# Optimization experiments

Measured on AMD Instinct MI355X. Metric: run time of the kernel, lower is better.

Reference implementation:

```python
import jax, jax.numpy as jnp
import numpy as np

B, L = 1024, 256
D = 64        # neighbor_interaction_feat_dim
TD = 100      # time_encoder.dim
NUM_NODES = 20000


def setup_inputs() -> dict:
    key = jax.random.key(0)
    ks = jax.random.split(key, 12)
    return {
        "src_ids": jax.random.randint(ks[0], (B, L), 0, NUM_NODES),
        "dst_ids": jax.random.randint(ks[1], (B, L), 0, NUM_NODES),
        "src_times": jax.random.uniform(ks[2], (B, L), jnp.float32),
        "dst_times": jax.random.uniform(ks[3], (B, L), jnp.float32),
        "node_times": jax.random.uniform(ks[4], (B,), jnp.float32) + 1.0,
        "num_nodes": NUM_NODES,
        # LTF time encoder: cos(t * w + b)
        "w_time": jax.random.normal(ks[5], (TD,), jnp.float32),
        "b_time": jax.random.normal(ks[6], (TD,), jnp.float32) * 0.1,
        # time_to_scalar: Linear(TD, 1)
        "w_ts": jax.random.normal(ks[7], (TD,), jnp.float32) / np.sqrt(TD),
        "b_ts": jnp.zeros((), jnp.float32),
        # MLP: Linear(1, D) -> ReLU -> Linear(D, D)
        "w1": jax.random.normal(ks[8], (D,), jnp.float32),
        "b1": jax.random.normal(ks[9], (D,), jnp.float32) * 0.1,
        "w2": jax.random.normal(ks[10], (D, D), jnp.float32) / np.sqrt(D),
        "b2": jax.random.normal(ks[11], (D,), jnp.float32) * 0.1,
    }


def _histogram(ids, num_nodes):
    # per-row count of each node id, with id==0 treated as padding (count 0)
    b = ids.shape[0]
    mask = (ids != 0).astype(jnp.float32)
    hist = jnp.zeros((b, num_nodes), jnp.float32)
    return hist.at[jnp.arange(b)[:, None], ids].add(mask)


def _time_weight(time_diff, w_time, b_time, w_ts, b_ts):
    # LTF: cos(t*w + b) -> Linear(TD,1) -> sigmoid, all fused elementwise+dot
    feat = jnp.cos(time_diff[..., None] * w_time + b_time)  # (B,L,TD)
    return jax.nn.sigmoid(feat @ w_ts + b_ts)               # (B,L)


def _mlp_sum(weighted_counts, w1, b1, w2, b2):
    # weighted_counts: (B,L,2) scalar counts -> Linear(1,D) -> ReLU -> Linear(D,D), sum over axis 2
    h = jax.nn.relu(weighted_counts[..., None] * w1 + b1)   # (B,L,2,D)
    return (h @ w2 + b2).sum(axis=2)                        # (B,L,D)


def reference(src_ids, dst_ids, src_times, dst_times, node_times, num_nodes,
              w_time, b_time, w_ts, b_ts, w1, b1, w2, b2):
    hist_src = _histogram(src_ids, num_nodes)  # (B,N)
    hist_dst = _histogram(dst_ids, num_nodes)

    c_ss = jnp.take_along_axis(hist_src, src_ids, axis=1)
    c_sd = jnp.take_along_axis(hist_dst, src_ids, axis=1)
    c_ds = jnp.take_along_axis(hist_src, dst_ids, axis=1)
    c_dd = jnp.take_along_axis(hist_dst, dst_ids, axis=1)

    src_counts = jnp.stack([c_ss, c_sd], axis=2)  # (B,L,2)
    dst_counts = jnp.stack([c_ds, c_dd], axis=2)

    src_w = _time_weight(node_times[:, None] - src_times, w_time, b_time, w_ts, b_ts)
    dst_w = _time_weight(node_times[:, None] - dst_times, w_time, b_time, w_ts, b_ts)

    src_features = _mlp_sum(src_counts * src_w[..., None], w1, b1, w2, b2)
    dst_features = _mlp_sum(dst_counts * dst_w[..., None], w1, b1, w2, b2)
    return src_features, dst_features
```

## Files before the change

kernel.cpp:

```cpp
#include <hip/hip_runtime.h>

#define BB 1024
#define LL 256
#define DD 64
#define TDIM 100

typedef _Float16 half8_t __attribute__((ext_vector_type(8)));
typedef float f32x4 __attribute__((ext_vector_type(4)));

__global__ __launch_bounds__(256, 3) void tni_kernel(
    const int* __restrict__ src_ids, const int* __restrict__ dst_ids,
    const float* __restrict__ src_tm, const float* __restrict__ dst_tm,
    const float* __restrict__ node_tm,
    const float* __restrict__ w_time, const float* __restrict__ b_time,
    const float* __restrict__ w_ts, const float* __restrict__ b_ts,
    const float* __restrict__ w1, const float* __restrict__ b1,
    const float* __restrict__ w2, const float* __restrict__ b2,
    float* __restrict__ out)
{
    __shared__ half8_t W2v[DD*8];
    __shared__ half8_t Gv[LL*8];

    const int t    = threadIdx.x;
    const int b    = blockIdx.x >> 1;
    const int side = blockIdx.x & 1;

    {
        _Float16* w2s = (_Float16*)W2v;
        #pragma unroll
        for (int i = 0; i < 16; ++i) {
            int idx = t + 256*i;
            int e = idx >> 6, d = idx & 63;
            int chunk = (e >> 3) ^ (d & 7);
            w2s[d*64 + (chunk << 3) + (e & 7)] = (_Float16)w2[idx];
        }
    }

    const int*   my_ids = side ? dst_ids : src_ids;
    const float* my_tms = side ? dst_tm  : src_tm;
    const int   my_id = my_ids[b*LL + t];
    const float my_tm = my_tms[b*LL + t];

    const int4* sr4 = (const int4*)(src_ids + b*LL);
    const int4* dr4 = (const int4*)(dst_ids + b*LL);
    int c1 = 0, c2 = 0;
    #pragma unroll 8
    for (int j = 0; j < LL/4; ++j) {
        int4 a  = sr4[j];
        int4 dd = dr4[j];
        c1 += (a.x==my_id) + (a.y==my_id) + (a.z==my_id) + (a.w==my_id);
        c2 += (dd.x==my_id) + (dd.y==my_id) + (dd.z==my_id) + (dd.w==my_id);
    }
    if (my_id == 0) { c1 = 0; c2 = 0; }

    const float inv2pi = 0.15915494309189535f;
    float td = node_tm[b] - my_tm;
    float z  = b_ts[0];
    #pragma unroll 4
    for (int k = 0; k < TDIM; ++k) {
        float u = fmaf(td, w_time[k], b_time[k]);
        float r = __builtin_amdgcn_fractf(u * inv2pi);
        z = fmaf(__builtin_amdgcn_cosf(r), w_ts[k], z);
    }
    float ee  = __builtin_amdgcn_exp2f(-1.44269504f * z);
    float wgt = __builtin_amdgcn_rcpf(1.0f + ee);
    float c1w = (float)c1 * wgt;
    float c2w = (float)c2 * wgt;

    #pragma unroll
    for (int c = 0; c < 8; ++c) {
        half8_t h;
        #pragma unroll
        for (int j = 0; j < 8; ++j) {
            float w1e = w1[c*8 + j], b1e = b1[c*8 + j];
            float g = fmaxf(fmaf(c1w, w1e, b1e), 0.f)
                    + fmaxf(fmaf(c2w, w1e, b1e), 0.f);
            h[j] = (_Float16)g;
        }
        Gv[t*8 + (c ^ (t & 7))] = h;
    }
    __syncthreads();

    const int w    = t >> 6;
    const int l    = t & 63;
    const int quad = l >> 4;
    const int lr   = l & 15;

    f32x4 acc[4][4];
    #pragma unroll
    for (int mt = 0; mt < 4; ++mt)
        #pragma unroll
        for (int nt = 0; nt < 4; ++nt) {
            f32x4 zz = {0.f, 0.f, 0.f, 0.f};
            acc[mt][nt] = zz;
        }

    #pragma unroll
    for (int s = 0; s < 2; ++s) {
        const int c = s*4 + quad;
        half8_t bfr[4], afr[4];
        #pragma unroll
        for (int nt = 0; nt < 4; ++nt) {
            int n = nt*16 + lr;
            bfr[nt] = W2v[n*8 + (c ^ (n & 7))];
        }
        #pragma unroll
        for (int mt = 0; mt < 4; ++mt) {
            int row = w*64 + mt*16 + lr;
            afr[mt] = Gv[row*8 + (c ^ (row & 7))];
        }
        #pragma unroll
        for (int mt = 0; mt < 4; ++mt)
            #pragma unroll
            for (int nt = 0; nt < 4; ++nt)
                acc[mt][nt] = __builtin_amdgcn_mfma_f32_16x16x32_f16(
                    afr[mt], bfr[nt], acc[mt][nt], 0, 0, 0);
    }

    float b2v[4];
    #pragma unroll
    for (int nt = 0; nt < 4; ++nt)
        b2v[nt] = 2.f * b2[nt*16 + lr];

    const int obase = side * (BB*LL*DD) + b * (LL*DD);
    #pragma unroll
    for (int mt = 0; mt < 4; ++mt) {
        #pragma unroll
        for (int r = 0; r < 4; ++r) {
            int pos = w*64 + mt*16 + quad*4 + r;
            #pragma unroll
            for (int nt = 0; nt < 4; ++nt) {
                out[obase + pos*DD + nt*16 + lr] = acc[mt][nt][r] + b2v[nt];
            }
        }
    }
}

extern "C" void kernel_launch(void* const* d_in, const int* in_sizes, int n_in,
                              void* d_out, int out_size, void* d_ws, size_t ws_size,
                              hipStream_t stream) {
    const int* src_ids = (const int*)d_in[0];
    const int* dst_ids = (const int*)d_in[1];
    const float* src_tm  = (const float*)d_in[2];
    const float* dst_tm  = (const float*)d_in[3];
    const float* node_tm = (const float*)d_in[4];
    const float* w_time = (const float*)d_in[6];
    const float* b_time = (const float*)d_in[7];
    const float* w_ts   = (const float*)d_in[8];
    const float* b_ts   = (const float*)d_in[9];
    const float* w1     = (const float*)d_in[10];
    const float* b1     = (const float*)d_in[11];
    const float* w2     = (const float*)d_in[12];
    const float* b2     = (const float*)d_in[13];
    float* out = (float*)d_out;

    tni_kernel<<<dim3(BB*2), dim3(256), 0, stream>>>(
        src_ids, dst_ids, src_tm, dst_tm, node_tm,
        w_time, b_time, w_ts, b_ts, w1, b1, w2, b2, out);
}
```

Measured before the change: 187.4 us.

## Replace MLP matmul with precomputed piecewise-linear breakpoint table lookup

```diff
diff --git a/kernel.cpp b/kernel.cpp
--- a/kernel.cpp
+++ b/kernel.cpp
@@ -5,36 +5,79 @@
 #define DD 64
 #define TDIM 100
 
-typedef _Float16 half8_t __attribute__((ext_vector_type(8)));
-typedef float f32x4 __attribute__((ext_vector_type(4)));
+#define BIG 3.0e38f
+#define TBL_OFF 256
 
-__global__ __launch_bounds__(256, 3) void tni_kernel(
+__global__ void tni_prep(const float* __restrict__ w1, const float* __restrict__ b1,
+                         const float* __restrict__ w2, const float* __restrict__ b2,
+                         float* __restrict__ ws)
+{
+    __shared__ float tauS[DD];
+    __shared__ int   vS[DD];
+    __shared__ float bpS[DD];
+    __shared__ int   beS[DD];
+
+    const int t = threadIdx.x;
+    float we = w1[t], be = b1[t];
+    float tau = -be / we;
+    int valid = (we != 0.0f) && (tau > 0.0f) && (tau < 1.0e3f);
+    tauS[t] = tau; vS[t] = valid;
+    bpS[t] = BIG;  beS[t] = 0;
+    __syncthreads();
+
+    int rank = 0;
+    for (int j = 0; j < DD; ++j) {
+        if (vS[j] && (tauS[j] < tau || (tauS[j] == tau && j < t))) rank++;
+    }
+    __syncthreads();
+    if (valid) { bpS[rank] = tau; beS[rank] = t; }
+    __syncthreads();
+
+    ws[t] = bpS[t];
+
+    float c0 = fminf(bpS[0] * 0.5f, 1.0f);
+    float A  = 0.0f;
+    float Bv = b2[t];
+    for (int e = 0; e < DD; ++e) {
+        float w1e = w1[e], b1e = b1[e];
+        float w2r = w2[e*DD + t];
+        if (fmaf(c0, w1e, b1e) > 0.0f) {
+            A  = fmaf(w1e, w2r, A);
+            Bv = fmaf(b1e, w2r, Bv);
+        }
+    }
+    float* tbl = ws + TBL_OFF;
+    tbl[(t>>2)*8     + (t&3)] = A;
+    tbl[(t>>2)*8 + 4 + (t&3)] = Bv;
+    for (int i = 0; i < DD; ++i) {
+        if (bpS[i] > 1.0e38f) break;
+        int   e   = beS[i];
+        float w1e = w1[e], b1e = b1[e];
+        float w2r = w2[e*DD + t];
+        float s   = (w1e > 0.0f) ? 1.0f : -1.0f;
+        A  = fmaf(s*w1e, w2r, A);
+        Bv = fmaf(s*b1e, w2r, Bv);
+        tbl[(i+1)*128 + (t>>2)*8     + (t&3)] = A;
+        tbl[(i+1)*128 + (t>>2)*8 + 4 + (t&3)] = Bv;
+    }
+}
+
+__global__ __launch_bounds__(256, 6) void tni_main(
     const int* __restrict__ src_ids, const int* __restrict__ dst_ids,
     const float* __restrict__ src_tm, const float* __restrict__ dst_tm,
     const float* __restrict__ node_tm,
     const float* __restrict__ w_time, const float* __restrict__ b_time,
     const float* __restrict__ w_ts, const float* __restrict__ b_ts,
-    const float* __restrict__ w1, const float* __restrict__ b1,
-    const float* __restrict__ w2, const float* __restrict__ b2,
-    float* __restrict__ out)
+    const float* __restrict__ ws, float* __restrict__ out)
 {
-    __shared__ half8_t W2v[DD*8];
-    __shared__ half8_t Gv[LL*8];
+    __shared__ float  bpS[DD];
+    __shared__ float4 cv[LL];
 
     const int t    = threadIdx.x;
     const int b    = blockIdx.x >> 1;
     const int side = blockIdx.x & 1;
 
-    {
-        _Float16* w2s = (_Float16*)W2v;
-        #pragma unroll
-        for (int i = 0; i < 16; ++i) {
-            int idx = t + 256*i;
-            int e = idx >> 6, d = idx & 63;
-            int chunk = (e >> 3) ^ (d & 7);
-            w2s[d*64 + (chunk << 3) + (e & 7)] = (_Float16)w2[idx];
-        }
-    }
+    if (t < DD) bpS[t] = ws[t];
 
     const int*   my_ids = side ? dst_ids : src_ids;
     const float* my_tms = side ? dst_tm  : src_tm;
@@ -44,7 +87,7 @@
     const int4* sr4 = (const int4*)(src_ids + b*LL);
     const int4* dr4 = (const int4*)(dst_ids + b*LL);
     int c1 = 0, c2 = 0;
-    #pragma unroll 8
+    #pragma unroll 2
     for (int j = 0; j < LL/4; ++j) {
         int4 a  = sr4[j];
         int4 dd = dr4[j];
@@ -67,72 +110,42 @@
     float c1w = (float)c1 * wgt;
     float c2w = (float)c2 * wgt;
 
-    #pragma unroll
-    for (int c = 0; c < 8; ++c) {
-        half8_t h;
-        #pragma unroll
-        for (int j = 0; j < 8; ++j) {
-            float w1e = w1[c*8 + j], b1e = b1[c*8 + j];
-            float g = fmaxf(fmaf(c1w, w1e, b1e), 0.f)
-                    + fmaxf(fmaf(c2w, w1e, b1e), 0.f);
-            h[j] = (_Float16)g;
-        }
-        Gv[t*8 + (c ^ (t & 7))] = h;
-    }
     __syncthreads();
 
-    const int w    = t >> 6;
-    const int l    = t & 63;
-    const int quad = l >> 4;
-    const int lr   = l & 15;
+    int k1 = 0, k2 = 0;
+    #pragma unroll
+    for (int s = 32; s >= 1; s >>= 1) {
+        k1 += (bpS[k1 + s - 1] < c1w) ? s : 0;
+        k2 += (bpS[k2 + s - 1] < c2w) ? s : 0;
+    }
+    k1 += (bpS[k1] < c1w) ? 1 : 0;
+    k2 += (bpS[k2] < c2w) ? 1 : 0;
 
-    f32x4 acc[4][4];
-    #pragma unroll
-    for (int mt = 0; mt < 4; ++mt)
-        #pragma unroll
-        for (int nt = 0; nt < 4; ++nt) {
-            f32x4 zz = {0.f, 0.f, 0.f, 0.f};
-            acc[mt][nt] = zz;
-        }
+    cv[t] = make_float4(c1w, c2w, __int_as_float(k1), __int_as_float(k2));
+    __syncthreads();
 
-    #pragma unroll
-    for (int s = 0; s < 2; ++s) {
-        const int c = s*4 + quad;
-        half8_t bfr[4], afr[4];
-        #pragma unroll
-        for (int nt = 0; nt < 4; ++nt) {
-            int n = nt*16 + lr;
-            bfr[nt] = W2v[n*8 + (c ^ (n & 7))];
-        }
-        #pragma unroll
-        for (int mt = 0; mt < 4; ++mt) {
-            int row = w*64 + mt*16 + lr;
-            afr[mt] = Gv[row*8 + (c ^ (row & 7))];
-        }
-        #pragma unroll
-        for (int mt = 0; mt < 4; ++mt)
-            #pragma unroll
-            for (int nt = 0; nt < 4; ++nt)
-                acc[mt][nt] = __builtin_amdgcn_mfma_f32_16x16x32_f16(
-                    afr[mt], bfr[nt], acc[mt][nt], 0, 0, 0);
-    }
+    const int w  = t >> 6;
+    const int l  = t & 63;
+    const int pq = l >> 4;
+    const int ch = l & 15;
+    const float* tbl = ws + TBL_OFF;
+    const int obase = side * (BB*LL*DD) + b * (LL*DD);
 
-    float b2v[4];
-    #pragma unroll
-    for (int nt = 0; nt < 4; ++nt)
-        b2v[nt] = 2.f * b2[nt*16 + lr];
-
-    const int obase = side * (BB*LL*DD) + b * (LL*DD);
-    #pragma unroll
-    for (int mt = 0; mt < 4; ++mt) {
-        #pragma unroll
-        for (int r = 0; r < 4; ++r) {
-            int pos = w*64 + mt*16 + quad*4 + r;
-            #pragma unroll
-            for (int nt = 0; nt < 4; ++nt) {
-                out[obase + pos*DD + nt*16 + lr] = acc[mt][nt][r] + b2v[nt];
-            }
-        }
+    #pragma unroll 4
+    for (int s = 0; s < 16; ++s) {
+        int p = w*64 + s*4 + pq;
+        float4 c = cv[p];
+        int ka = __float_as_int(c.z), kb = __float_as_int(c.w);
+        const float4* r1 = (const float4*)(tbl + ka*128 + ch*8);
+        const float4* r2 = (const float4*)(tbl + kb*128 + ch*8);
+        float4 A1 = r1[0], B1 = r1[1];
+        float4 A2 = r2[0], B2 = r2[1];
+        float4 o;
+        o.x = fmaf(c.x, A1.x, B1.x) + fmaf(c.y, A2.x, B2.x);
+        o.y = fmaf(c.x, A1.y, B1.y) + fmaf(c.y, A2.y, B2.y);
+        o.z = fmaf(c.x, A1.z, B1.z) + fmaf(c.y, A2.z, B2.z);
+        o.w = fmaf(c.x, A1.w, B1.w) + fmaf(c.y, A2.w, B2.w);
+        *(float4*)(out + obase + p*DD + ch*4) = o;
     }
 }
 
@@ -153,8 +166,10 @@
     const float* w2     = (const float*)d_in[12];
     const float* b2     = (const float*)d_in[13];
     float* out = (float*)d_out;
+    float* ws  = (float*)d_ws;
 
-    tni_kernel<<<dim3(BB*2), dim3(256), 0, stream>>>(
+    tni_prep<<<dim3(1), dim3(64), 0, stream>>>(w1, b1, w2, b2, ws);
+    tni_main<<<dim3(BB*2), dim3(256), 0, stream>>>(
         src_ids, dst_ids, src_tm, dst_tm, node_tm,
-        w_time, b_time, w_ts, b_ts, w1, b1, w2, b2, out);
+        w_time, b_time, w_ts, b_ts, ws, out);
 }
```

New measurement: 213.8 us. 14.1% more time.
